# Optimization experiments

Hardware: AMD Instinct MI355X
Metric: run time of the kernel (lower is better)

The kernel has to match this reference:

```python
import jax, jax.numpy as jnp
import numpy as np

N_NODES = 50000
N_EDGES = 800000
IN_F = 128
OUT_F = 128
EDGE_F = 6


def setup_inputs() -> dict:
    key = jax.random.key(0)
    k1, k2, k3, k4, k5, k6, k7 = jax.random.split(key, 7)
    nodeFeatures = jax.random.normal(k1, (N_NODES, IN_F), dtype=jnp.float32)
    edgeIndex = jax.random.randint(k2, (N_EDGES, 2), 0, N_NODES, dtype=jnp.int64)
    edgeFeatures = jax.random.normal(k3, (N_EDGES, EDGE_F), dtype=jnp.float32)
    # nn.Linear params (kaiming-uniform-ish init scale)
    lim_n = 1.0 / np.sqrt(IN_F)
    lim_e = 1.0 / np.sqrt(EDGE_F)
    W = jax.random.uniform(k4, (IN_F, OUT_F), minval=-lim_n, maxval=lim_n, dtype=jnp.float32)
    b = jax.random.uniform(k5, (OUT_F,), minval=-lim_n, maxval=lim_n, dtype=jnp.float32)
    We = jax.random.uniform(k6, (EDGE_F, OUT_F), minval=-lim_e, maxval=lim_e, dtype=jnp.float32)
    be = jax.random.uniform(k7, (OUT_F,), minval=-lim_e, maxval=lim_e, dtype=jnp.float32)
    return {"nodeFeatures": nodeFeatures, "edgeIndex": edgeIndex,
            "edgeFeatures": edgeFeatures, "W": W, "b": b, "We": We, "be": be}


def reference(nodeFeatures, edgeIndex, edgeFeatures, W, b, We, be):
    # node linear: [N, out]
    transformed = nodeFeatures @ W + b
    # edge linear: [E, out]
    edgeMsg = edgeFeatures @ We + be
    src = edgeIndex[:, 0]
    dst = edgeIndex[:, 1]
    # per-edge message = transformed[src] + edgeMsg, scatter-add into dst
    messages = transformed[src] + edgeMsg  # [E, out]
    aggregated = jax.ops.segment_sum(messages, dst, num_segments=nodeFeatures.shape[0])
    return jax.nn.relu(aggregated)
```

## Files before the change

kernel.cpp:

```cpp
#include <hip/hip_runtime.h>
#include <hip/hip_bf16.h>
#include <stdint.h>

#define IN_F 128
#define EDGE_F 6
#define TILE_E 4096
#define NBIN_PAD 256
#define BCAP 8192
#define CAST_B 400

using bf16x8 = __attribute__((ext_vector_type(8))) short;
using f32x4  = __attribute__((ext_vector_type(4))) float;

__device__ __forceinline__ float bf2f(unsigned short u) {
    return __uint_as_float(((unsigned int)u) << 16);
}
__device__ __forceinline__ unsigned short f2bfbits(float f) {
    __hip_bfloat16 h = __float2bfloat16(f);
    return *reinterpret_cast<unsigned short*>(&h);
}
__device__ __forceinline__ unsigned int packbf(float a, float b) {
    return ((unsigned int)f2bfbits(b) << 16) | (unsigned int)f2bfbits(a);
}

__global__ __launch_bounds__(256) void sort_pack_cast(
        const int* __restrict__ eidx, const float* __restrict__ ef,
        uint4* __restrict__ rec_c, unsigned short* __restrict__ pmat,
        unsigned short* __restrict__ lmat,
        int n_edges, int nblk_e, int n_cast, int n_nodes,
        const float* __restrict__ nf, unsigned short* __restrict__ nfb,
        const float* __restrict__ W, const float* __restrict__ b,
        const float* __restrict__ We, const float* __restrict__ be,
        unsigned short* __restrict__ Wpack, float* __restrict__ W2pack) {
    const int tid = threadIdx.x;
    const int blk = blockIdx.x;
    __shared__ unsigned int qxs[TILE_E];
    __shared__ int hist[NBIN_PAD];
    __shared__ int cur[NBIN_PAD];

    if (blk < nblk_e) {
        hist[tid] = 0;
        __syncthreads();
        const int e0 = blk * TILE_E;
        const int lim = min(TILE_E, n_edges - e0);
        for (int i = tid; i < lim; i += 256) {
            const int2 pr = reinterpret_cast<const int2*>(eidx)[e0 + i];
            const unsigned int q = (unsigned int)pr.x | ((unsigned int)pr.y << 16);
            qxs[i] = q;
            atomicAdd(&hist[q >> 24], 1);
        }
        __syncthreads();
        const int own = hist[tid];
        for (int off = 1; off < 256; off <<= 1) {
            int t2 = (tid >= off) ? hist[tid - off] : 0;
            __syncthreads();
            hist[tid] += t2;
            __syncthreads();
        }
        const int excl = hist[tid] - own;
        pmat[(size_t)blk * NBIN_PAD + tid] = (unsigned short)own;
        lmat[(size_t)blk * NBIN_PAD + tid] = (unsigned short)excl;
        cur[tid] = excl;
        __syncthreads();
        uint4* seg = rec_c + (size_t)blk * TILE_E;
        for (int i = tid; i < lim; i += 256) {
            const unsigned int q = qxs[i];
            const float2* efs = reinterpret_cast<const float2*>(ef + (size_t)(e0 + i) * EDGE_F);
            const float2 f0 = efs[0], f1 = efs[1], f2 = efs[2];
            uint4 r;
            r.x = q;
            r.y = packbf(f0.x, f0.y);
            r.z = packbf(f1.x, f1.y);
            r.w = packbf(f2.x, f2.y);
            const int pos = atomicAdd(&cur[q >> 24], 1);
            seg[pos] = r;
        }
    } else if (blk == nblk_e) {
        for (int idx = tid; idx < 16384; idx += 256) {
            int j = idx & 7, lane = (idx >> 3) & 63, ft = (idx >> 9) & 7, kb = idx >> 12;
            int k = kb * 32 + (lane >> 4) * 8 + j;
            int f = ft * 16 + (lane & 15);
            Wpack[idx] = f2bfbits(W[k * 128 + f]);
        }
        for (int idx = tid; idx < 1024; idx += 256) {
            int j = idx >> 7, f = idx & 127;
            float w = 0.f;
            if (j < 6)       w = We[j * 128 + f];
            else if (j == 6) w = b[f] + be[f];
            W2pack[idx] = w;
        }
        if (tid < 16) {
            uint4 z; z.x = z.y = z.z = z.w = 0u;
            reinterpret_cast<uint4*>(nfb + (size_t)n_nodes * IN_F)[tid] = z;
        }
    } else {
        const int cb = blk - nblk_e - 1;
        const int ncb = gridDim.x - nblk_e - 1;
        for (int i = cb * 256 + tid; i < n_cast; i += ncb * 256) {
            const float4 lo = reinterpret_cast<const float4*>(nf)[2 * i];
            const float4 hi = reinterpret_cast<const float4*>(nf)[2 * i + 1];
            uint4 o;
            o.x = packbf(lo.x, lo.y); o.y = packbf(lo.z, lo.w);
            o.z = packbf(hi.x, hi.y); o.w = packbf(hi.z, hi.w);
            reinterpret_cast<uint4*>(nfb)[i] = o;
        }
    }
}

__global__ __launch_bounds__(256) void fine_rank(
        const uint4* __restrict__ rec_c, const unsigned short* __restrict__ pmat,
        const unsigned short* __restrict__ lmat,
        uint4* __restrict__ rec, int2* __restrict__ pr2,
        int n_nodes, int nblk_e) {
    const int tid = threadIdx.x;
    const int c = blockIdx.x;
    __shared__ int fcnt[256];
    __shared__ int fpos[256];
    const int cnt_t = (tid < nblk_e) ? pmat[(size_t)tid * NBIN_PAD + c] : 0;
    const int ofs_t = (tid < nblk_e) ? lmat[(size_t)tid * NBIN_PAD + c] : 0;
    const uint4* runp = rec_c + (size_t)tid * TILE_E + ofs_t;
    fcnt[tid] = 0;
    __syncthreads();
    for (int k = 0; k < cnt_t; ++k) {
        const unsigned int qx = reinterpret_cast<const unsigned int*>(runp)[4 * k];
        atomicAdd(&fcnt[(qx >> 16) & 255], 1);
    }
    __syncthreads();
    const int own = fcnt[tid];
    const int ownp = (own + 7) & ~7;
    fcnt[tid] = ownp;
    __syncthreads();
    for (int off = 1; off < 256; off <<= 1) {
        int t2 = (tid >= off) ? fcnt[tid - off] : 0;
        __syncthreads();
        fcnt[tid] += t2;
        __syncthreads();
    }
    const int pexcl = fcnt[tid] - ownp;
    fpos[tid] = pexcl;
    const size_t obase = (size_t)c * BCAP;
    const int n = c * 256 + tid;
    if (n < n_nodes) {
        int2 pr; pr.x = (int)(obase + pexcl); pr.y = own;
        pr2[n] = pr;
    }
    __syncthreads();
    for (int k = 0; k < cnt_t; ++k) {
        const uint4 q = runp[k];
        const int r = atomicAdd(&fpos[(q.x >> 16) & 255], 1);
        if (r < BCAP) rec[obase + r] = q;
    }
    uint4 dmy; dmy.x = (unsigned int)n_nodes; dmy.y = dmy.z = dmy.w = 0u;
    for (int j = own; j < ownp && pexcl + j < BCAP; ++j)
        rec[obase + pexcl + j] = dmy;
}

__global__ __launch_bounds__(256) void aggregate_bf16(
        const unsigned short* __restrict__ nfb, const uint4* __restrict__ rec,
        const int2* __restrict__ pr2, unsigned short* __restrict__ S,
        unsigned short* __restrict__ E8, int n_nodes) {
    const int lane = threadIdx.x & 63;
    const int wv = __builtin_amdgcn_readfirstlane(threadIdx.x >> 6);
    const int n = blockIdx.x * 4 + wv;
    if (n >= n_nodes) return;
    const int2 pr = pr2[n];
    const int deg = pr.y;
    const int nb = (deg + 7) >> 3;
    const int half = lane >> 5;
    const int hl = lane & 31;
    float a0 = 0.f, a1 = 0.f, a2 = 0.f, a3 = 0.f;
    float e0 = 0.f, e1 = 0.f, e2 = 0.f, e3 = 0.f, e4 = 0.f, e5 = 0.f;
    int i = pr.x;
    for (int bb = 0; bb < nb; ++bb, i += 8) {
        uint4 q[8];
#pragma unroll
        for (int j = 0; j < 8; ++j) q[j] = rec[i + j];
        uint2 u[4];
#pragma unroll
        for (int p = 0; p < 4; ++p) {
            const unsigned int sA = q[2 * p].x & 0xFFFFu;
            const unsigned int sB = q[2 * p + 1].x & 0xFFFFu;
            const unsigned int s = half ? sB : sA;
            u[p] = reinterpret_cast<const uint2*>(nfb + (size_t)s * IN_F)[hl];
        }
#pragma unroll
        for (int p = 0; p < 4; ++p) {
            a0 += bf2f((unsigned short)u[p].x);
            a1 += bf2f((unsigned short)(u[p].x >> 16));
            a2 += bf2f((unsigned short)u[p].y);
            a3 += bf2f((unsigned short)(u[p].y >> 16));
        }
#pragma unroll
        for (int j = 0; j < 8; ++j) {
            e0 += bf2f((unsigned short)q[j].y);
            e1 += bf2f((unsigned short)(q[j].y >> 16));
            e2 += bf2f((unsigned short)q[j].z);
            e3 += bf2f((unsigned short)(q[j].z >> 16));
            e4 += bf2f((unsigned short)q[j].w);
            e5 += bf2f((unsigned short)(q[j].w >> 16));
        }
    }
    a0 += __shfl_xor(a0, 32, 64);
    a1 += __shfl_xor(a1, 32, 64);
    a2 += __shfl_xor(a2, 32, 64);
    a3 += __shfl_xor(a3, 32, 64);
    if (half == 0) {
        uint2 o;
        o.x = packbf(a0, a1);
        o.y = packbf(a2, a3);
        reinterpret_cast<uint2*>(S + (size_t)n * IN_F)[hl] = o;
    }
    if (lane == 0) {
        uint4 q;
        q.x = packbf(e0, e1);
        q.y = packbf(e2, e3);
        q.z = packbf(e4, e5);
        q.w = packbf((float)deg, 0.f);
        *reinterpret_cast<uint4*>(E8 + (size_t)n * 8) = q;
    }
}

__global__ __launch_bounds__(256) void gemm_mfma(
        const unsigned short* __restrict__ S, const unsigned short* __restrict__ E8,
        const unsigned short* __restrict__ Wpack, const float* __restrict__ W2pack,
        float* __restrict__ out, int n_nodes) {
    __shared__ __align__(16) short Wl[16384];
    __shared__ float W2l[1024];
    const int tid = threadIdx.x;
    for (int i = tid; i < 2048; i += 256)
        reinterpret_cast<uint4*>(Wl)[i] = reinterpret_cast<const uint4*>(Wpack)[i];
    for (int i = tid; i < 1024; i += 256) W2l[i] = W2pack[i];

    const int wv = tid >> 6, lane = tid & 63;
    const int m = lane & 15, quad = lane >> 4;
    const int n0 = blockIdx.x * 64 + wv * 16;

    const int arow = min(n0 + m, n_nodes - 1);
    const unsigned short* ap = S + (size_t)arow * IN_F + quad * 8;
    bf16x8 a[4];
#pragma unroll
    for (int kb = 0; kb < 4; ++kb)
        a[kb] = *reinterpret_cast<const bf16x8*>(ap + kb * 32);

    __syncthreads();

    f32x4 acc[8];
#pragma unroll
    for (int ft = 0; ft < 8; ++ft) acc[ft] = (f32x4){0.f, 0.f, 0.f, 0.f};

#pragma unroll
    for (int kb = 0; kb < 4; ++kb) {
#pragma unroll
        for (int ft = 0; ft < 8; ++ft) {
            const bf16x8 bfrag =
                reinterpret_cast<const bf16x8*>(Wl)[(kb * 8 + ft) * 64 + lane];
            acc[ft] = __builtin_amdgcn_mfma_f32_16x16x32_bf16(a[kb], bfrag, acc[ft], 0, 0, 0);
        }
    }

    float e[4][7];
#pragma unroll
    for (int r = 0; r < 4; ++r) {
        const int n = min(n0 + quad * 4 + r, n_nodes - 1);
        const uint4 q = *reinterpret_cast<const uint4*>(E8 + (size_t)n * 8);
        e[r][0] = bf2f((unsigned short)q.x); e[r][1] = bf2f((unsigned short)(q.x >> 16));
        e[r][2] = bf2f((unsigned short)q.y); e[r][3] = bf2f((unsigned short)(q.y >> 16));
        e[r][4] = bf2f((unsigned short)q.z); e[r][5] = bf2f((unsigned short)(q.z >> 16));
        e[r][6] = bf2f((unsigned short)q.w);
    }
#pragma unroll
    for (int ft = 0; ft < 8; ++ft) {
        const int f = ft * 16 + m;
        float w2[7];
#pragma unroll
        for (int j = 0; j < 7; ++j) w2[j] = W2l[j * 128 + f];
#pragma unroll
        for (int r = 0; r < 4; ++r) {
            const int n = n0 + quad * 4 + r;
            if (n < n_nodes) {
                float v = acc[ft][r];
#pragma unroll
                for (int j = 0; j < 7; ++j) v += e[r][j] * w2[j];
                out[(size_t)n * 128 + f] = fmaxf(v, 0.f);
            }
        }
    }
}

extern "C" void kernel_launch(void* const* d_in, const int* in_sizes, int n_in,
                              void* d_out, int out_size, void* d_ws, size_t ws_size,
                              hipStream_t stream) {
    const float* nf = (const float*)d_in[0];
    const int* eidx = (const int*)d_in[1];
    const float* ef = (const float*)d_in[2];
    const float* W  = (const float*)d_in[3];
    const float* b  = (const float*)d_in[4];
    const float* We = (const float*)d_in[5];
    const float* be = (const float*)d_in[6];
    float* out = (float*)d_out;

    const int n_nodes = in_sizes[0] / IN_F;
    const int n_edges = in_sizes[1] / 2;

    const int nblk_e = (n_edges + TILE_E - 1) / TILE_E;
    const int nbin = (n_nodes + 255) >> 8;
    const int n_cast = n_nodes * (IN_F / 8);

    uint4* rec   = (uint4*)d_ws;
    uint4* rec_c = rec + (size_t)nbin * BCAP;
    unsigned short* S = (unsigned short*)(rec_c + (size_t)nblk_e * TILE_E);
    unsigned short* E8 = S + (size_t)n_nodes * IN_F;
    unsigned short* Wpack = E8 + (size_t)n_nodes * 8;
    float* W2pack = (float*)(Wpack + 16384);
    int2* pr2 = (int2*)(W2pack + 1024);
    unsigned short* pmat = (unsigned short*)(pr2 + n_nodes);
    unsigned short* lmat = pmat + (size_t)nblk_e * NBIN_PAD;
    unsigned short* nfb = lmat + (size_t)nblk_e * NBIN_PAD;

    sort_pack_cast<<<nblk_e + 1 + CAST_B, 256, 0, stream>>>(
        eidx, ef, rec_c, pmat, lmat, n_edges, nblk_e, n_cast, n_nodes,
        nf, nfb, W, b, We, be, Wpack, W2pack);
    fine_rank<<<nbin, 256, 0, stream>>>(rec_c, pmat, lmat, rec, pr2,
                                        n_nodes, nblk_e);
    aggregate_bf16<<<(n_nodes + 3) / 4, 256, 0, stream>>>(nfb, rec, pr2, S, E8, n_nodes);
    gemm_mfma<<<(n_nodes + 63) / 64, 256, 0, stream>>>(S, E8, Wpack, W2pack, out, n_nodes);
}
```

Measured before the change: 195.4 us.

## Flatten fine_rank work across 512 threads and stage gemm output through LDS

fine_rank previously gave each thread one edge-tile run, so it looped serially over a variable number of records. Now a 512-thread block builds a prefix over the run lengths and binary-searches each flat record index into its run. This spreads the records evenly across threads and caches the gathered indices in shared memory, which adds a 32 KB LDS array. It also truncates a bin at IDXN records, so a bin holding more than that many edges would lose some. Separately, the gemm epilogue writes results into shared memory and then stores full 16-byte rows to output, replacing strided scalar stores.

```diff
diff --git a/kernel.cpp b/kernel.cpp
--- a/kernel.cpp
+++ b/kernel.cpp
@@ -7,6 +7,7 @@
 #define TILE_E 4096
 #define NBIN_PAD 256
 #define BCAP 8192
+#define IDXN 8192
 #define CAST_B 400
 
 using bf16x8 = __attribute__((ext_vector_type(8))) short;
@@ -107,52 +108,108 @@
     }
 }
 
-__global__ __launch_bounds__(256) void fine_rank(
+__global__ __launch_bounds__(512) void fine_rank(
         const uint4* __restrict__ rec_c, const unsigned short* __restrict__ pmat,
         const unsigned short* __restrict__ lmat,
         uint4* __restrict__ rec, int2* __restrict__ pr2,
         int n_nodes, int nblk_e) {
     const int tid = threadIdx.x;
     const int c = blockIdx.x;
+    __shared__ int rstart[NBIN_PAD + 1];
+    __shared__ int rbaseg[NBIN_PAD];
     __shared__ int fcnt[256];
     __shared__ int fpos[256];
-    const int cnt_t = (tid < nblk_e) ? pmat[(size_t)tid * NBIN_PAD + c] : 0;
-    const int ofs_t = (tid < nblk_e) ? lmat[(size_t)tid * NBIN_PAD + c] : 0;
-    const uint4* runp = rec_c + (size_t)tid * TILE_E + ofs_t;
-    fcnt[tid] = 0;
-    __syncthreads();
-    for (int k = 0; k < cnt_t; ++k) {
-        const unsigned int qx = reinterpret_cast<const unsigned int*>(runp)[4 * k];
-        atomicAdd(&fcnt[(qx >> 16) & 255], 1);
-    }
-    __syncthreads();
-    const int own = fcnt[tid];
-    const int ownp = (own + 7) & ~7;
-    fcnt[tid] = ownp;
+    __shared__ int idxl[IDXN];
+
+    if (tid < 256) {
+        const bool r = (tid < nblk_e);
+        fcnt[tid] = r ? pmat[(size_t)tid * NBIN_PAD + c] : 0;
+        rbaseg[tid] = tid * TILE_E + (r ? (int)lmat[(size_t)tid * NBIN_PAD + c] : 0);
+    }
     __syncthreads();
     for (int off = 1; off < 256; off <<= 1) {
-        int t2 = (tid >= off) ? fcnt[tid - off] : 0;
-        __syncthreads();
-        fcnt[tid] += t2;
-        __syncthreads();
-    }
-    const int pexcl = fcnt[tid] - ownp;
-    fpos[tid] = pexcl;
+        int v = 0;
+        if (tid < 256 && tid >= off) v = fcnt[tid - off];
+        __syncthreads();
+        if (tid < 256) fcnt[tid] += v;
+        __syncthreads();
+    }
+    if (tid < 256) rstart[tid + 1] = fcnt[tid];
+    if (tid == 0) rstart[0] = 0;
+    __syncthreads();
+    int sz = rstart[256];
+    if (sz > IDXN) sz = IDXN;
+    __syncthreads();
+    if (tid < 256) fcnt[tid] = 0;
+    __syncthreads();
+    for (int base = 0; base < sz; base += 2048) {
+        int ii[4], g[4];
+        unsigned int qx[4];
+#pragma unroll
+        for (int u = 0; u < 4; ++u) ii[u] = base + u * 512 + tid;
+#pragma unroll
+        for (int u = 0; u < 4; ++u) {
+            if (ii[u] < sz) {
+                int lo = 0, hi = 255;
+                while (lo < hi) {
+                    const int mid = (lo + hi + 1) >> 1;
+                    if (rstart[mid] <= ii[u]) lo = mid; else hi = mid - 1;
+                }
+                g[u] = rbaseg[lo] + (ii[u] - rstart[lo]);
+                idxl[ii[u]] = g[u];
+            }
+        }
+#pragma unroll
+        for (int u = 0; u < 4; ++u)
+            if (ii[u] < sz)
+                qx[u] = reinterpret_cast<const unsigned int*>(rec_c)[(size_t)g[u] * 4];
+#pragma unroll
+        for (int u = 0; u < 4; ++u)
+            if (ii[u] < sz) atomicAdd(&fcnt[(qx[u] >> 16) & 255], 1);
+    }
+    __syncthreads();
+    int own = 0, ownp = 0, pexcl = 0;
+    if (tid < 256) { own = fcnt[tid]; ownp = (own + 7) & ~7; fcnt[tid] = ownp; }
+    __syncthreads();
+    for (int off = 1; off < 256; off <<= 1) {
+        int v = 0;
+        if (tid < 256 && tid >= off) v = fcnt[tid - off];
+        __syncthreads();
+        if (tid < 256) fcnt[tid] += v;
+        __syncthreads();
+    }
     const size_t obase = (size_t)c * BCAP;
-    const int n = c * 256 + tid;
-    if (n < n_nodes) {
-        int2 pr; pr.x = (int)(obase + pexcl); pr.y = own;
-        pr2[n] = pr;
-    }
-    __syncthreads();
-    for (int k = 0; k < cnt_t; ++k) {
-        const uint4 q = runp[k];
-        const int r = atomicAdd(&fpos[(q.x >> 16) & 255], 1);
-        if (r < BCAP) rec[obase + r] = q;
-    }
-    uint4 dmy; dmy.x = (unsigned int)n_nodes; dmy.y = dmy.z = dmy.w = 0u;
-    for (int j = own; j < ownp && pexcl + j < BCAP; ++j)
-        rec[obase + pexcl + j] = dmy;
+    if (tid < 256) {
+        pexcl = fcnt[tid] - ownp;
+        fpos[tid] = pexcl;
+        const int n = c * 256 + tid;
+        if (n < n_nodes) {
+            int2 pr; pr.x = (int)(obase + pexcl); pr.y = own;
+            pr2[n] = pr;
+        }
+    }
+    __syncthreads();
+    for (int base = 0; base < sz; base += 2048) {
+        int ii[4];
+        uint4 q[4];
+#pragma unroll
+        for (int u = 0; u < 4; ++u) ii[u] = base + u * 512 + tid;
+#pragma unroll
+        for (int u = 0; u < 4; ++u)
+            if (ii[u] < sz) q[u] = rec_c[idxl[ii[u]]];
+#pragma unroll
+        for (int u = 0; u < 4; ++u) {
+            if (ii[u] < sz) {
+                const int r = atomicAdd(&fpos[(q[u].x >> 16) & 255], 1);
+                if (r < BCAP) rec[obase + r] = q[u];
+            }
+        }
+    }
+    if (tid < 256) {
+        uint4 dmy; dmy.x = (unsigned int)n_nodes; dmy.y = dmy.z = dmy.w = 0u;
+        for (int j = own; j < ownp && pexcl + j < BCAP; ++j)
+            rec[obase + pexcl + j] = dmy;
+    }
 }
 
 __global__ __launch_bounds__(256) void aggregate_bf16(
@@ -268,6 +325,8 @@
         e[r][4] = bf2f((unsigned short)q.z); e[r][5] = bf2f((unsigned short)(q.z >> 16));
         e[r][6] = bf2f((unsigned short)q.w);
     }
+    __syncthreads();
+    float* So = reinterpret_cast<float*>(Wl);
 #pragma unroll
     for (int ft = 0; ft < 8; ++ft) {
         const int f = ft * 16 + m;
@@ -276,14 +335,19 @@
         for (int j = 0; j < 7; ++j) w2[j] = W2l[j * 128 + f];
 #pragma unroll
         for (int r = 0; r < 4; ++r) {
-            const int n = n0 + quad * 4 + r;
-            if (n < n_nodes) {
-                float v = acc[ft][r];
-#pragma unroll
-                for (int j = 0; j < 7; ++j) v += e[r][j] * w2[j];
-                out[(size_t)n * 128 + f] = fmaxf(v, 0.f);
-            }
-        }
+            float v = acc[ft][r];
+#pragma unroll
+            for (int j = 0; j < 7; ++j) v += e[r][j] * w2[j];
+            So[(wv * 16 + quad * 4 + r) * 128 + f] = fmaxf(v, 0.f);
+        }
+    }
+    __syncthreads();
+    const size_t nb0 = (size_t)blockIdx.x * 64;
+    for (int i = tid; i < 2048; i += 256) {
+        const int row = i >> 5;
+        if (nb0 + row < (size_t)n_nodes)
+            reinterpret_cast<uint4*>(out)[(nb0 + row) * 32 + (i & 31)] =
+                reinterpret_cast<const uint4*>(So)[i];
     }
 }
 
@@ -320,7 +384,7 @@
     sort_pack_cast<<<nblk_e + 1 + CAST_B, 256, 0, stream>>>(
         eidx, ef, rec_c, pmat, lmat, n_edges, nblk_e, n_cast, n_nodes,
         nf, nfb, W, b, We, be, Wpack, W2pack);
-    fine_rank<<<nbin, 256, 0, stream>>>(rec_c, pmat, lmat, rec, pr2,
+    fine_rank<<<nbin, 512, 0, stream>>>(rec_c, pmat, lmat, rec, pr2,
                                         n_nodes, nblk_e);
     aggregate_bf16<<<(n_nodes + 3) / 4, 256, 0, stream>>>(nfb, rec, pr2, S, E8, n_nodes);
     gemm_mfma<<<(n_nodes + 63) / 64, 256, 0, stream>>>(S, E8, Wpack, W2pack, out, n_nodes);
```

Result: faster. 177.6 us (median of 2 runs) (-9.1%).
